# Performance work log

Hardware: AMD Instinct MI355X
Metric: run time of the kernel (lower is better)

Reference implementation:

```python
import jax, jax.numpy as jnp
import numpy as np

DIM = 2048
N_EXPERTS = 8
TOP_K = 2


def setup_inputs() -> dict:
    key = jax.random.key(0)
    ks = jax.random.split(key, 5)
    x = jax.random.normal(ks[0], (4, 4096, DIM), dtype=jnp.float32)
    # Linear(dim, dim, bias=False) stores weight as [out, in]; y = x @ W.T
    W_up = jax.random.normal(ks[1], (DIM, DIM), dtype=jnp.float32) * (1.0 / np.sqrt(DIM))
    W_down = jax.random.normal(ks[2], (DIM, DIM), dtype=jnp.float32) * (1.0 / np.sqrt(DIM))
    W_gate = jax.random.normal(ks[3], (N_EXPERTS, DIM), dtype=jnp.float32) * (1.0 / np.sqrt(DIM))
    # expert_weight: nn.Parameter(torch.randn(dim, dim)), applied as x @ W_expert
    W_expert = jax.random.normal(ks[4], (DIM, DIM), dtype=jnp.float32) * (1.0 / np.sqrt(DIM))
    return {"x": x, "W_up": W_up, "W_down": W_down, "W_gate": W_gate, "W_expert": W_expert}


def reference(x, W_up, W_down, W_gate, W_expert):
    # Gating: logits [B,S,E], top-k routing
    logits = jnp.einsum("bsd,ed->bse", x, W_gate)
    routing_weights, selected_experts = jax.lax.top_k(logits, TOP_K)  # [B,S,K]
    # Shared expert MLP
    shared_out = jnp.einsum("bsd,od->bso", jax.nn.relu(jnp.einsum("bsd,od->bso", x, W_up)), W_down)
    # Mock MoE combine: all selected experts share a single weight matrix, so the
    # dispatch-compute-scatter collapses to a softmax-normalized weighted sum of the
    # same expert output per token (weights sum to 1 over k).
    rw = jax.nn.softmax(routing_weights, axis=-1)  # [B,S,K]
    expert_out = jnp.einsum("bsd,do->bso", x, W_expert)  # shared across selected experts
    moe_out = jnp.sum(rw, axis=-1, keepdims=True) * expert_out
    return shared_out + moe_out
```

## Files before the change

### kernel.cpp

```cpp
#include <hip/hip_runtime.h>
#include <hip/hip_bf16.h>
#include <stdint.h>


#define DIM 2048
#define MTOT 16384

typedef unsigned short u16;
typedef __bf16 bf16x8 __attribute__((ext_vector_type(8)));
typedef float f32x4 __attribute__((ext_vector_type(4)));

__device__ __forceinline__ u16 f2bf(float f) {
    union { float f; unsigned int u; } a; a.f = f;
    unsigned int u = a.u;
    unsigned int r = (u + 0x7fffu + ((u >> 16) & 1u)) >> 16;
    return (u16)r;
}

__device__ __forceinline__ bf16x8 frag_load(const void* p) {
    union { uint4 u; bf16x8 b; } x;
    x.u = *(const uint4*)p;
    return x.b;
}

__global__ void cvt_pack(const float* __restrict__ src, u16* __restrict__ dst,
                         long n4, int dld, int doff) {
    long i = (long)blockIdx.x * blockDim.x + threadIdx.x;
    long stride = (long)gridDim.x * blockDim.x;
    for (; i < n4; i += stride) {
        long e = i << 2;
        long row = e >> 11;
        int col = (int)(e & 2047);
        float4 v = *(const float4*)(src + e);
        union { u16 q[4]; uint2 d; } u;
        u.q[0] = f2bf(v.x); u.q[1] = f2bf(v.y);
        u.q[2] = f2bf(v.z); u.q[3] = f2bf(v.w);
        *(uint2*)(dst + row * (long)dld + doff + col) = u.d;
    }
}

__global__ void cvt_transpose(const float* __restrict__ W, u16* __restrict__ dst) {
    __shared__ float t[32][33];
    int bx = blockIdx.x & 63;
    int by = blockIdx.x >> 6;
    int x = threadIdx.x & 31, y = threadIdx.x >> 5;
    #pragma unroll
    for (int j = 0; j < 32; j += 8)
        t[y + j][x] = W[(size_t)(by * 32 + y + j) * 2048 + bx * 32 + x];
    __syncthreads();
    #pragma unroll
    for (int j = 0; j < 32; j += 8)
        dst[(size_t)(bx * 32 + y + j) * 4096 + 2048 + by * 32 + x] = f2bf(t[x][y + j]);
}

template <int MODE>
__global__ __launch_bounds__(512, 2)
void gemm256(const u16* __restrict__ A, const u16* __restrict__ B,
             void* __restrict__ Cptr, int lda, int ldb, int K) {
    __shared__ char lds[2][65536];

    const int tid  = threadIdx.x;
    const int lane = tid & 63;
    const int wv   = tid >> 6;
    const int wr   = wv >> 2;
    const int wc   = wv & 3;

    int bid = blockIdx.x;
    int cpx = gridDim.x >> 3;
    int swz = (bid & 7) * cpx + (bid >> 3);
    int tile_n = swz & 7;
    int tile_m = swz >> 3;

    const int rowA0 = tile_m * 256;
    const int rowB0 = tile_n * 256;

    const int r_sub = tid >> 3;
    const int c_src = ((tid & 7) ^ (r_sub & 7)) << 3;
    const u16* pAb = A + (size_t)(rowA0 + r_sub) * lda + c_src;
    const u16* pBb = B + (size_t)(rowB0 + r_sub) * ldb + c_src;

    f32x4 acc[2][2][4][2];
    #pragma unroll
    for (int a = 0; a < 2; ++a)
        #pragma unroll
        for (int b = 0; b < 2; ++b)
            #pragma unroll
            for (int m = 0; m < 4; ++m)
                #pragma unroll
                for (int n = 0; n < 2; ++n)
                    acc[a][b][m][n] = (f32x4){0.f, 0.f, 0.f, 0.f};

    bf16x8 av[4][2];
    bf16x8 bva[2][2];
    bf16x8 bvb[2][2];
    const int kA = (lane >> 4) << 4;

#define STAGE_A(H, KOFF, BUF) do {                                              \
    const u16* _s = pAb + (size_t)((H) * 128) * lda + (KOFF);                   \
    __builtin_amdgcn_global_load_lds(                                           \
        (const __attribute__((address_space(1))) void*)_s,                      \
        (__attribute__((address_space(3))) void*)((char*)lds[BUF] + (H)*16384 + (wv<<10)), \
        16, 0, 0);                                                              \
    __builtin_amdgcn_global_load_lds(                                           \
        (const __attribute__((address_space(1))) void*)(_s + (size_t)64 * lda), \
        (__attribute__((address_space(3))) void*)((char*)lds[BUF] + (H)*16384 + 8192 + (wv<<10)), \
        16, 0, 0);                                                              \
  } while (0)

#define STAGE_B(H, KOFF, BUF) do {                                              \
    const u16* _s = pBb + (size_t)((H) * 128) * ldb + (KOFF);                   \
    __builtin_amdgcn_global_load_lds(                                           \
        (const __attribute__((address_space(1))) void*)_s,                      \
        (__attribute__((address_space(3))) void*)((char*)lds[BUF] + 32768 + (H)*16384 + (wv<<10)), \
        16, 0, 0);                                                              \
    __builtin_amdgcn_global_load_lds(                                           \
        (const __attribute__((address_space(1))) void*)(_s + (size_t)64 * ldb), \
        (__attribute__((address_space(3))) void*)((char*)lds[BUF] + 32768 + (H)*16384 + 8192 + (wv<<10)), \
        16, 0, 0);                                                              \
  } while (0)

#define DSREAD_A(MH, CUR) do {                                                  \
    _Pragma("unroll")                                                           \
    for (int m = 0; m < 4; ++m) {                                               \
        int ra = (wr << 6) + (m << 4) + (lane & 15);                            \
        const char* _b = (const char*)lds[CUR] + (MH)*16384 + (ra << 7);        \
        int sw = (ra & 7) << 4;                                                 \
        av[m][0] = frag_load(_b + (kA ^ sw));                                   \
        av[m][1] = frag_load(_b + ((64 + kA) ^ sw));                            \
    } } while (0)

#define DSREAD_B(NH, CUR, DST) do {                                             \
    _Pragma("unroll")                                                           \
    for (int n = 0; n < 2; ++n) {                                               \
        int rb = (wc << 5) + (n << 4) + (lane & 15);                            \
        const char* _b = (const char*)lds[CUR] + 32768 + (NH)*16384 + (rb << 7);\
        int sw = (rb & 7) << 4;                                                 \
        DST[n][0] = frag_load(_b + (kA ^ sw));                                  \
        DST[n][1] = frag_load(_b + ((64 + kA) ^ sw));                           \
    } } while (0)

#define MFMA_Q(MH, NH, BV) do {                                                 \
    __builtin_amdgcn_s_setprio(1);                                              \
    _Pragma("unroll")                                                           \
    for (int m = 0; m < 4; ++m)                                                 \
        _Pragma("unroll")                                                       \
        for (int n = 0; n < 2; ++n) {                                           \
            acc[MH][NH][m][n] = __builtin_amdgcn_mfma_f32_16x16x32_bf16(        \
                av[m][0], BV[n][0], acc[MH][NH][m][n], 0, 0, 0);                \
            acc[MH][NH][m][n] = __builtin_amdgcn_mfma_f32_16x16x32_bf16(        \
                av[m][1], BV[n][1], acc[MH][NH][m][n], 0, 0, 0);                \
        }                                                                       \
    __builtin_amdgcn_s_setprio(0);                                              \
  } while (0)

#define WAIT_VM(N) asm volatile("s_waitcnt vmcnt(" #N ")" ::: "memory")
#define WAIT_LGKM0() asm volatile("s_waitcnt lgkmcnt(0)" ::: "memory")
#define BAR() __builtin_amdgcn_s_barrier()

    STAGE_A(0, 0, 0);
    STAGE_B(0, 0, 0);
    STAGE_B(1, 0, 0);
    STAGE_A(1, 0, 0);
    WAIT_VM(2);
    BAR();

    const int nK = K >> 6;
    int cur = 0;
    for (int t = 0; t < nK - 1; ++t) {
        const int koff = (t + 1) << 6;
        const int nxt = cur ^ 1;
        DSREAD_B(0, cur, bva);
        DSREAD_B(1, cur, bvb);
        DSREAD_A(0, cur);
        STAGE_A(0, koff, nxt);
        STAGE_B(0, koff, nxt);
        MFMA_Q(0, 0, bva);
        MFMA_Q(0, 1, bvb);
        WAIT_LGKM0();
        WAIT_VM(4);
        BAR();
        DSREAD_A(1, cur);
        STAGE_B(1, koff, nxt);
        STAGE_A(1, koff, nxt);
        MFMA_Q(1, 1, bvb);
        MFMA_Q(1, 0, bva);
        WAIT_LGKM0();
        WAIT_VM(2);
        BAR();
        cur = nxt;
    }

    DSREAD_B(0, cur, bva);
    DSREAD_B(1, cur, bvb);
    DSREAD_A(0, cur);
    MFMA_Q(0, 0, bva);
    MFMA_Q(0, 1, bvb);
    WAIT_LGKM0();
    WAIT_VM(0);
    BAR();
    DSREAD_A(1, cur);
    MFMA_Q(1, 1, bvb);
    MFMA_Q(1, 0, bva);

    #pragma unroll
    for (int mh = 0; mh < 2; ++mh)
        #pragma unroll
        for (int m = 0; m < 4; ++m)
            #pragma unroll
            for (int r = 0; r < 4; ++r) {
                int row = rowA0 + mh * 128 + (wr << 6) + (m << 4) + ((lane >> 4) << 2) + r;
                #pragma unroll
                for (int nh = 0; nh < 2; ++nh)
                    #pragma unroll
                    for (int n = 0; n < 2; ++n) {
                        int col = tile_n * 256 + nh * 128 + (wc << 5) + (n << 4) + (lane & 15);
                        float v = acc[mh][nh][m][n][r];
                        if (MODE == 0) {
                            ((u16*)Cptr)[(size_t)row * 4096 + col] = f2bf(fmaxf(v, 0.f));
                        } else {
                            ((float*)Cptr)[(size_t)row * 2048 + col] = v;
                        }
                    }
            }
#undef STAGE_A
#undef STAGE_B
#undef DSREAD_A
#undef DSREAD_B
#undef MFMA_Q
#undef WAIT_VM
#undef WAIT_LGKM0
#undef BAR
}

extern "C" void kernel_launch(void* const* d_in, const int* in_sizes, int n_in,
                              void* d_out, int out_size, void* d_ws, size_t ws_size,
                              hipStream_t stream) {
    const float* x        = (const float*)d_in[0];
    const float* W_up     = (const float*)d_in[1];
    const float* W_down   = (const float*)d_in[2];
    const float* W_expert = (const float*)d_in[4];

    u16* Abig = (u16*)d_ws;
    u16* Bbig = Abig + (size_t)MTOT * 4096;
    u16* Wup  = Bbig + (size_t)DIM * 4096;

    cvt_pack<<<2048, 256, 0, stream>>>(x, Abig, (long)MTOT * DIM / 4, 4096, 2048);
    cvt_pack<<<1024, 256, 0, stream>>>(W_up, Wup, (long)DIM * DIM / 4, 2048, 0);
    cvt_pack<<<1024, 256, 0, stream>>>(W_down, Bbig, (long)DIM * DIM / 4, 4096, 0);
    cvt_transpose<<<4096, 256, 0, stream>>>(W_expert, Bbig);

    gemm256<0><<<512, 512, 0, stream>>>(Abig + 2048, Wup, Abig, 4096, 2048, 2048);
    gemm256<1><<<512, 512, 0, stream>>>(Abig, Bbig, d_out, 4096, 4096, 4096);
}
```

Measured before the change: 369.2 us.

## Switch GEMM to 32x32x16 MFMA and simplify double-buffered K loop

Replaces the 16x16x32 bf16 MFMA tiling with 32x32x16 MFMA fragments, so each wave issues fewer, larger matrix instructions and performs fewer LDS fragment reads per unit of work. The fine-grained two-phase pipeline, with partial vmcnt waits and a mid-iteration barrier, is replaced by a single phase: issue all next-tile global-to-LDS loads, compute the whole current tile, then wait for all loads and take one barrier. This reduces LDS read traffic and instruction count. In exchange it loses the interleaving of compute with half-tile loads, and it reads LDS without explicit lgkm waits, relying on the compiler to insert them.

```diff
diff --git a/kernel.cpp b/kernel.cpp
--- a/kernel.cpp
+++ b/kernel.cpp
@@ -8,7 +8,7 @@
 
 typedef unsigned short u16;
 typedef __bf16 bf16x8 __attribute__((ext_vector_type(8)));
-typedef float f32x4 __attribute__((ext_vector_type(4)));
+typedef float f32x16 __attribute__((ext_vector_type(16)));
 
 __device__ __forceinline__ u16 f2bf(float f) {
     union { float f; unsigned int u; } a; a.f = f;
@@ -79,21 +79,16 @@
     const u16* pAb = A + (size_t)(rowA0 + r_sub) * lda + c_src;
     const u16* pBb = B + (size_t)(rowB0 + r_sub) * ldb + c_src;
 
-    f32x4 acc[2][2][4][2];
-    #pragma unroll
-    for (int a = 0; a < 2; ++a)
+    f32x16 acc[4][2];
+    #pragma unroll
+    for (int m = 0; m < 4; ++m)
         #pragma unroll
-        for (int b = 0; b < 2; ++b)
-            #pragma unroll
-            for (int m = 0; m < 4; ++m)
-                #pragma unroll
-                for (int n = 0; n < 2; ++n)
-                    acc[a][b][m][n] = (f32x4){0.f, 0.f, 0.f, 0.f};
-
-    bf16x8 av[4][2];
-    bf16x8 bva[2][2];
-    bf16x8 bvb[2][2];
-    const int kA = (lane >> 4) << 4;
+        for (int n = 0; n < 2; ++n)
+            acc[m][n] = (f32x16)0.f;
+
+    bf16x8 av[4], bv[2];
+    const int laneR = lane & 31;
+    const int kHalf = (lane >> 5) << 4;
 
 #define STAGE_A(H, KOFF, BUF) do {                                              \
     const u16* _s = pAb + (size_t)((H) * 128) * lda + (KOFF);                   \
@@ -119,49 +114,41 @@
         16, 0, 0);                                                              \
   } while (0)
 
-#define DSREAD_A(MH, CUR) do {                                                  \
+#define TILE_COMPUTE(CUR) do {                                                  \
+    const char* _base = (const char*)lds[CUR];                                  \
     _Pragma("unroll")                                                           \
-    for (int m = 0; m < 4; ++m) {                                               \
-        int ra = (wr << 6) + (m << 4) + (lane & 15);                            \
-        const char* _b = (const char*)lds[CUR] + (MH)*16384 + (ra << 7);        \
-        int sw = (ra & 7) << 4;                                                 \
-        av[m][0] = frag_load(_b + (kA ^ sw));                                   \
-        av[m][1] = frag_load(_b + ((64 + kA) ^ sw));                            \
-    } } while (0)
-
-#define DSREAD_B(NH, CUR, DST) do {                                             \
-    _Pragma("unroll")                                                           \
-    for (int n = 0; n < 2; ++n) {                                               \
-        int rb = (wc << 5) + (n << 4) + (lane & 15);                            \
-        const char* _b = (const char*)lds[CUR] + 32768 + (NH)*16384 + (rb << 7);\
-        int sw = (rb & 7) << 4;                                                 \
-        DST[n][0] = frag_load(_b + (kA ^ sw));                                  \
-        DST[n][1] = frag_load(_b + ((64 + kA) ^ sw));                           \
-    } } while (0)
-
-#define MFMA_Q(MH, NH, BV) do {                                                 \
-    __builtin_amdgcn_s_setprio(1);                                              \
-    _Pragma("unroll")                                                           \
-    for (int m = 0; m < 4; ++m)                                                 \
+    for (int ks = 0; ks < 4; ++ks) {                                            \
+        const int kb = (ks << 5) + kHalf;                                       \
         _Pragma("unroll")                                                       \
         for (int n = 0; n < 2; ++n) {                                           \
-            acc[MH][NH][m][n] = __builtin_amdgcn_mfma_f32_16x16x32_bf16(        \
-                av[m][0], BV[n][0], acc[MH][NH][m][n], 0, 0, 0);                \
-            acc[MH][NH][m][n] = __builtin_amdgcn_mfma_f32_16x16x32_bf16(        \
-                av[m][1], BV[n][1], acc[MH][NH][m][n], 0, 0, 0);                \
+            int rb = (wc << 5) + laneR;                                         \
+            bv[n] = frag_load(_base + 32768 + n * 16384 + (rb << 7)             \
+                              + (kb ^ ((rb & 7) << 4)));                        \
         }                                                                       \
-    __builtin_amdgcn_s_setprio(0);                                              \
-  } while (0)
-
-#define WAIT_VM(N) asm volatile("s_waitcnt vmcnt(" #N ")" ::: "memory")
-#define WAIT_LGKM0() asm volatile("s_waitcnt lgkmcnt(0)" ::: "memory")
+        _Pragma("unroll")                                                       \
+        for (int mf = 0; mf < 4; ++mf) {                                        \
+            int ra = (wr << 6) + ((mf & 1) << 5) + laneR;                       \
+            av[mf] = frag_load(_base + (mf >> 1) * 16384 + (ra << 7)            \
+                               + (kb ^ ((ra & 7) << 4)));                       \
+        }                                                                       \
+        __builtin_amdgcn_s_setprio(1);                                          \
+        _Pragma("unroll")                                                       \
+        for (int mf = 0; mf < 4; ++mf)                                          \
+            _Pragma("unroll")                                                   \
+            for (int n = 0; n < 2; ++n)                                         \
+                acc[mf][n] = __builtin_amdgcn_mfma_f32_32x32x16_bf16(           \
+                    av[mf], bv[n], acc[mf][n], 0, 0, 0);                        \
+        __builtin_amdgcn_s_setprio(0);                                          \
+    } } while (0)
+
+#define WAIT_VM0() asm volatile("s_waitcnt vmcnt(0)" ::: "memory")
 #define BAR() __builtin_amdgcn_s_barrier()
 
     STAGE_A(0, 0, 0);
     STAGE_B(0, 0, 0);
     STAGE_B(1, 0, 0);
     STAGE_A(1, 0, 0);
-    WAIT_VM(2);
+    WAIT_VM0();
     BAR();
 
     const int nK = K >> 6;
@@ -169,66 +156,40 @@
     for (int t = 0; t < nK - 1; ++t) {
         const int koff = (t + 1) << 6;
         const int nxt = cur ^ 1;
-        DSREAD_B(0, cur, bva);
-        DSREAD_B(1, cur, bvb);
-        DSREAD_A(0, cur);
         STAGE_A(0, koff, nxt);
         STAGE_B(0, koff, nxt);
-        MFMA_Q(0, 0, bva);
-        MFMA_Q(0, 1, bvb);
-        WAIT_LGKM0();
-        WAIT_VM(4);
-        BAR();
-        DSREAD_A(1, cur);
         STAGE_B(1, koff, nxt);
         STAGE_A(1, koff, nxt);
-        MFMA_Q(1, 1, bvb);
-        MFMA_Q(1, 0, bva);
-        WAIT_LGKM0();
-        WAIT_VM(2);
+        TILE_COMPUTE(cur);
+        WAIT_VM0();
         BAR();
         cur = nxt;
     }
-
-    DSREAD_B(0, cur, bva);
-    DSREAD_B(1, cur, bvb);
-    DSREAD_A(0, cur);
-    MFMA_Q(0, 0, bva);
-    MFMA_Q(0, 1, bvb);
-    WAIT_LGKM0();
-    WAIT_VM(0);
-    BAR();
-    DSREAD_A(1, cur);
-    MFMA_Q(1, 1, bvb);
-    MFMA_Q(1, 0, bva);
-
-    #pragma unroll
-    for (int mh = 0; mh < 2; ++mh)
+    TILE_COMPUTE(cur);
+
+    #pragma unroll
+    for (int mf = 0; mf < 4; ++mf) {
+        int rbase = rowA0 + (mf >> 1) * 128 + (wr << 6) + ((mf & 1) << 5)
+                    + ((lane >> 5) << 2);
         #pragma unroll
-        for (int m = 0; m < 4; ++m)
+        for (int n = 0; n < 2; ++n) {
+            int col = tile_n * 256 + n * 128 + (wc << 5) + laneR;
             #pragma unroll
-            for (int r = 0; r < 4; ++r) {
-                int row = rowA0 + mh * 128 + (wr << 6) + (m << 4) + ((lane >> 4) << 2) + r;
-                #pragma unroll
-                for (int nh = 0; nh < 2; ++nh)
-                    #pragma unroll
-                    for (int n = 0; n < 2; ++n) {
-                        int col = tile_n * 256 + nh * 128 + (wc << 5) + (n << 4) + (lane & 15);
-                        float v = acc[mh][nh][m][n][r];
-                        if (MODE == 0) {
-                            ((u16*)Cptr)[(size_t)row * 4096 + col] = f2bf(fmaxf(v, 0.f));
-                        } else {
-                            ((float*)Cptr)[(size_t)row * 2048 + col] = v;
-                        }
-                    }
+            for (int reg = 0; reg < 16; ++reg) {
+                int row = rbase + (reg & 3) + ((reg >> 2) << 3);
+                float v = acc[mf][n][reg];
+                if (MODE == 0) {
+                    ((u16*)Cptr)[(size_t)row * 4096 + col] = f2bf(fmaxf(v, 0.f));
+                } else {
+                    ((float*)Cptr)[(size_t)row * 2048 + col] = v;
+                }
             }
+        }
+    }
 #undef STAGE_A
 #undef STAGE_B
-#undef DSREAD_A
-#undef DSREAD_B
-#undef MFMA_Q
-#undef WAIT_VM
-#undef WAIT_LGKM0
+#undef TILE_COMPUTE
+#undef WAIT_VM0
 #undef BAR
 }
 
```

New measurement: 464.4 us. 1.26x slower.

## Reschedule GEMM main loop into four barrier-separated phases; fuse conversion kernels

Applied to the files above, without the earlier changes.

The K-loop of the 256x256 bf16 MFMA GEMM now interleaves LDS reads, global staging and MFMA quarters with barriers, lgkmcnt waits and sched_barriers between each quarter, in a ping-pong style schedule meant to overlap memory and matrix work more tightly. The three fp32-to-bf16 pack launches are merged into one grid-stride kernel to cut launch overhead. The extra barriers add synchronisation cost, and the changed vmcnt thresholds must still line up with the staging order for correctness.

```diff
diff --git a/kernel.cpp b/kernel.cpp
--- a/kernel.cpp
+++ b/kernel.cpp
@@ -23,12 +23,18 @@
     return x.b;
 }
 
-__global__ void cvt_pack(const float* __restrict__ src, u16* __restrict__ dst,
-                         long n4, int dld, int doff) {
+__global__ void cvt_all(const float* __restrict__ x, const float* __restrict__ Wu,
+                        const float* __restrict__ Wd, u16* __restrict__ Abig,
+                        u16* __restrict__ Wup, u16* __restrict__ Bbig) {
+    const long NX = (long)MTOT * DIM / 4;
+    const long NW = (long)DIM * DIM / 4;
     long i = (long)blockIdx.x * blockDim.x + threadIdx.x;
     long stride = (long)gridDim.x * blockDim.x;
-    for (; i < n4; i += stride) {
-        long e = i << 2;
+    for (; i < NX + 2 * NW; i += stride) {
+        const float* src; u16* dst; int dld, doff; long e;
+        if (i < NX)            { src = x;  dst = Abig; dld = 4096; doff = 2048; e = i << 2; }
+        else if (i < NX + NW)  { src = Wu; dst = Wup;  dld = 2048; doff = 0;    e = (i - NX) << 2; }
+        else                   { src = Wd; dst = Bbig; dld = 4096; doff = 0;    e = (i - NX - NW) << 2; }
         long row = e >> 11;
         int col = (int)(e & 2047);
         float4 v = *(const float4*)(src + e);
@@ -154,14 +160,17 @@
   } while (0)
 
 #define WAIT_VM(N) asm volatile("s_waitcnt vmcnt(" #N ")" ::: "memory")
-#define WAIT_LGKM0() asm volatile("s_waitcnt lgkmcnt(0)" ::: "memory")
+#define LG() do {                                                               \
+    asm volatile("s_waitcnt lgkmcnt(0)" ::: "memory");                          \
+    __builtin_amdgcn_sched_barrier(0);                                          \
+  } while (0)
 #define BAR() __builtin_amdgcn_s_barrier()
 
     STAGE_A(0, 0, 0);
     STAGE_B(0, 0, 0);
     STAGE_B(1, 0, 0);
     STAGE_A(1, 0, 0);
-    WAIT_VM(2);
+    WAIT_VM(4);
     BAR();
 
     const int nK = K >> 6;
@@ -169,36 +178,38 @@
     for (int t = 0; t < nK - 1; ++t) {
         const int koff = (t + 1) << 6;
         const int nxt = cur ^ 1;
+        DSREAD_A(0, cur);
         DSREAD_B(0, cur, bva);
+        STAGE_A(0, koff, nxt);
+        WAIT_VM(4); BAR(); LG();
+        MFMA_Q(0, 0, bva);
+        BAR();
         DSREAD_B(1, cur, bvb);
-        DSREAD_A(0, cur);
-        STAGE_A(0, koff, nxt);
         STAGE_B(0, koff, nxt);
-        MFMA_Q(0, 0, bva);
+        WAIT_VM(4); BAR(); LG();
         MFMA_Q(0, 1, bvb);
-        WAIT_LGKM0();
-        WAIT_VM(4);
         BAR();
         DSREAD_A(1, cur);
         STAGE_B(1, koff, nxt);
+        BAR(); LG();
+        MFMA_Q(1, 1, bvb);
+        BAR();
         STAGE_A(1, koff, nxt);
-        MFMA_Q(1, 1, bvb);
+        WAIT_VM(4); BAR(); LG();
         MFMA_Q(1, 0, bva);
-        WAIT_LGKM0();
-        WAIT_VM(2);
         BAR();
         cur = nxt;
     }
 
+    DSREAD_A(0, cur);
     DSREAD_B(0, cur, bva);
+    WAIT_VM(2); BAR(); LG();
+    MFMA_Q(0, 0, bva);
     DSREAD_B(1, cur, bvb);
-    DSREAD_A(0, cur);
-    MFMA_Q(0, 0, bva);
+    WAIT_VM(0); LG();
     MFMA_Q(0, 1, bvb);
-    WAIT_LGKM0();
-    WAIT_VM(0);
-    BAR();
     DSREAD_A(1, cur);
+    LG();
     MFMA_Q(1, 1, bvb);
     MFMA_Q(1, 0, bva);
 
@@ -228,7 +239,7 @@
 #undef DSREAD_B
 #undef MFMA_Q
 #undef WAIT_VM
-#undef WAIT_LGKM0
+#undef LG
 #undef BAR
 }
 
@@ -244,9 +255,7 @@
     u16* Bbig = Abig + (size_t)MTOT * 4096;
     u16* Wup  = Bbig + (size_t)DIM * 4096;
 
-    cvt_pack<<<2048, 256, 0, stream>>>(x, Abig, (long)MTOT * DIM / 4, 4096, 2048);
-    cvt_pack<<<1024, 256, 0, stream>>>(W_up, Wup, (long)DIM * DIM / 4, 2048, 0);
-    cvt_pack<<<1024, 256, 0, stream>>>(W_down, Bbig, (long)DIM * DIM / 4, 4096, 0);
+    cvt_all<<<2048, 256, 0, stream>>>(x, W_up, W_down, Abig, Wup, Bbig);
     cvt_transpose<<<4096, 256, 0, stream>>>(W_expert, Bbig);
 
     gemm256<0><<<512, 512, 0, stream>>>(Abig + 2048, Wup, Abig, 4096, 2048, 2048);
```

New measurement: 398.1 us. +7.8%, slower.
